# Kernel tuning notes

Hardware: AMD Instinct MI355X
Metric: run time of the kernel (lower is better)

## Reference

```python
import jax, jax.numpy as jnp
import numpy as np

B, T, D_OBS = 64, 512, 128
D_LAT, D_HID, K = 16, 256, 8
VAR = 0.0005
LOG2PI = float(np.log(2.0 * np.pi))


def _leaky(x):
    return jnp.where(x > 0, x, 0.01 * x)


def setup_inputs() -> dict:
    key = jax.random.key(0)
    ks = jax.random.split(key, 12)
    s = 0.05
    return {
        "x": jax.random.normal(ks[0], (B, T, D_OBS), jnp.float32),
        "eps": jax.random.normal(ks[1], (B, T, D_LAT), jnp.float32),
        "W1": jax.random.normal(ks[2], (D_OBS, D_HID), jnp.float32) * s,
        "b1": jnp.zeros((D_HID,), jnp.float32),
        "W2": jax.random.normal(ks[3], (D_HID, 2 * D_LAT), jnp.float32) * s,
        "b2": jnp.zeros((2 * D_LAT,), jnp.float32),
        "Wt1": jax.random.normal(ks[4], (K, D_LAT, D_HID), jnp.float32) * s,
        "bt1": jnp.zeros((K, D_HID), jnp.float32),
        "Wt2": jax.random.normal(ks[5], (K, D_HID, D_LAT), jnp.float32) * s,
        "bt2": jnp.zeros((K, D_LAT), jnp.float32),
        "Wd1": jax.random.normal(ks[6], (D_LAT, D_HID), jnp.float32) * s,
        "bd1": jnp.zeros((D_HID,), jnp.float32),
        "Wd2": jax.random.normal(ks[7], (D_HID, D_OBS), jnp.float32) * s,
        "bd2": jnp.zeros((D_OBS,), jnp.float32),
        "Q": jax.random.normal(ks[8], (K, K), jnp.float32) * 0.1,
        "pi": jax.random.normal(ks[9], (K,), jnp.float32) * 0.1,
        "init_mean": jax.random.normal(ks[10], (K, D_LAT), jnp.float32),
        "init_cov": jax.random.uniform(ks[11], (K, 1, 1), jnp.float32) * jnp.eye(D_LAT, dtype=jnp.float32)[None] * 5.0,
        "covs": jnp.tile(jnp.eye(D_LAT, dtype=jnp.float32)[None], (K, 1, 1)),
    }


def _mvn_logprob(diff, chol):
    # diff [..., K, d]; chol [K, d, d] lower Cholesky of per-state covariance
    d = chol.shape[-1]
    Linv = jax.scipy.linalg.solve_triangular(
        chol, jnp.broadcast_to(jnp.eye(d, dtype=chol.dtype), chol.shape), lower=True)
    sol = jnp.einsum('kij,...kj->...ki', Linv, diff)
    logdet = 2.0 * jnp.sum(jnp.log(jnp.diagonal(chol, axis1=-2, axis2=-1)), -1)  # [K]
    return -0.5 * (d * LOG2PI + logdet + jnp.sum(sol * sol, -1))


def _forward(x, eps, W1, b1, W2, b2, Wt1, bt1, Wt2, bt2, Wd1, bd1, Wd2, bd2,
             Q, pi, init_mean, init_cov, covs):
    Bx = x.shape[0]
    dz = init_mean.shape[-1]
    # ---- factored MLP encoder: x -> (mu, logvar); reparameterized sample ----
    h = _leaky(x @ W1 + b1)
    enc = h @ W2 + b2
    z_mu, z_log_var = enc[..., :dz], enc[..., dz:]
    z = z_mu + jnp.exp(0.5 * z_log_var) * eps                            # [B,T,dz]
    # ---- local evidence log p(z_t | z_{t-1}, s_t=k) ----
    jitter = 1e-6 * jnp.eye(dz, dtype=x.dtype)
    L0 = jnp.linalg.cholesky(init_cov @ jnp.swapaxes(init_cov, -1, -2) + jitter)
    ev1 = _mvn_logprob(z[:, 0:1, None, :] - init_mean[None, None], L0)   # [B,1,K]
    ht = jax.nn.softplus(jnp.einsum('btd,kdh->btkh', z[:, :-1], Wt1) + bt1)
    means = jnp.einsum('btkh,khd->btkd', ht, Wt2) + bt2                  # [B,T-1,K,dz]
    Lt = jnp.linalg.cholesky(covs @ jnp.swapaxes(covs, -1, -2) + jitter)
    evT = _mvn_logprob(z[:, 1:, None, :] - means, Lt)                    # [B,T-1,K]
    ev = jnp.concatenate([ev1, evT], axis=1)                             # [B,T,K]
    # ---- HMM alpha recursion in log domain (temperature=1) ----
    log_pi = jax.nn.log_softmax(pi)
    Qlog = jax.nn.log_softmax(Q, axis=-1).T                              # [new, old]
    lp0 = ev[:, 0] + log_pi
    lZ0 = jax.scipy.special.logsumexp(lp0, axis=-1)
    la0 = lp0 - lZ0[:, None]

    def step(la, ev_t):
        lp = jax.scipy.special.logsumexp(ev_t[:, :, None] + Qlog[None] + la[:, None, :], axis=-1)
        lZ = jax.scipy.special.logsumexp(lp, axis=-1)
        return lp - lZ[:, None], lZ

    _, lZs = jax.lax.scan(step, la0, jnp.moveaxis(ev[:, 1:], 1, 0))
    log_Z = lZ0 + jnp.sum(lZs, axis=0)                                   # [B]
    # ---- decoder ----
    x_hat = _leaky(z @ Wd1 + bd1) @ Wd2 + bd2
    # ---- ELBO ----
    recon = jnp.sum(-0.5 * jnp.log(2.0 * jnp.pi * VAR) - (x - x_hat) ** 2 / (2.0 * VAR)) / Bx
    logq = -0.5 * (dz * LOG2PI + jnp.sum(z_log_var, -1)
                   + jnp.sum((z - z_mu) ** 2 / jnp.exp(z_log_var), -1))
    entropy_q = -jnp.sum(logq) / Bx
    msm = jnp.sum(log_Z) / Bx
    loss = -(recon + entropy_q + msm)
    return x_hat, z, loss


def reference(x, eps, W1, b1, W2, b2, Wt1, bt1, Wt2, bt2, Wd1, bd1, Wd2, bd2,
              Q, pi, init_mean, init_cov, covs):
    return _forward(x, eps, W1, b1, W2, b2, Wt1, bt1, Wt2, bt2, Wd1, bd1, Wd2, bd2,
                    Q, pi, init_mean, init_cov, covs)
```

## Files before the change

### kernel.cpp

```cpp
#include <hip/hip_runtime.h>
#include <math.h>

#define B_SZ   64
#define T_SZ   512
#define DOBS   128
#define DLAT   16
#define DHID   256
#define K_SZ   8
#define ROWS_A 32768

#define LOG2PI_F 1.8378770664093453f
#define VAR_F    5.0e-4f

#define LINV0_OFF   16
#define LOGDET0_OFF 2064
#define LINVT_OFF   2080
#define LOGDETT_OFF 4128
#define CVEC_OFF    4224
#define WIMG_F_OFF  8192

#define EVT_W1   0
#define EVT_W2   49152
#define EVT_LINV 82944
#define ENC_W1   86016
#define ENC_W2   120832
#define DEC_W1   129280
#define DEC_W2   135424
#define WCVT_TOTAL 182272

#define Z_OUT_OFF   4194304
#define LOSS_OFF    4718592
#define PBUF_OFF  262144
#define ACC_OFF   327680

typedef __attribute__((ext_vector_type(8))) short short8;
typedef __attribute__((ext_vector_type(8))) unsigned short ush8;
typedef __attribute__((ext_vector_type(4))) float floatx4;

__device__ __forceinline__ float leakyf(float v) { return v > 0.f ? v : 0.01f * v; }
__device__ __forceinline__ unsigned short f2bf(float f) {
  union { float f; unsigned int u; } v; v.f = f;
  unsigned int lsb = (v.u >> 16) & 1;
  v.u += 0x7fffu + lsb;
  return (unsigned short)(v.u >> 16);
}
__device__ __forceinline__ unsigned int cvt_pk_bf16(float lo, float hi) {
  unsigned int r;
  asm("v_cvt_pk_bf16_f32 %0, %1, %2" : "=v"(r) : "v"(lo), "v"(hi));
  return r;
}
__device__ __forceinline__ float softplus5(float v) {
  return 0.69314718f * __log2f(1.f + exp2f(1.44269504f * v));
}
__device__ __forceinline__ int permk(int kk) {
  return (kk & ~31) | ((kk & 15) << 1) | ((kk >> 4) & 1);
}

__global__ __launch_bounds__(256) void prep_kernel(const float* __restrict__ init_cov,
                                                   const float* __restrict__ covs,
                                                   const float* __restrict__ Wt2,
                                                   const float* __restrict__ bt2,
                                                   float* __restrict__ ws,
                                                   float* __restrict__ w2l) {
  __shared__ float M[16][16];
  __shared__ float L[16][16];
  __shared__ float X[16][17];
  int job = blockIdx.x;
  const float* C = (job < 8) ? (init_cov + job * 256) : (covs + (job - 8) * 256);
  float* linv = ws + ((job < 8) ? (LINV0_OFF + job * 256) : (LINVT_OFF + (job - 8) * 256));
  float* logdet = ws + ((job < 8) ? (LOGDET0_OFF + job) : (LOGDETT_OFF + (job - 8)));
  int tid = threadIdx.x;
  if (job == 0 && tid < 4) ws[tid] = 0.f;
  int i = tid >> 4, j = tid & 15;
  {
    float s = (i == j) ? 1e-6f : 0.f;
    #pragma unroll
    for (int p = 0; p < 16; ++p) s += C[i * 16 + p] * C[j * 16 + p];
    M[i][j] = s;
  }
  __syncthreads();
  for (int c = 0; c < 16; ++c) {
    if (tid == 0) {
      float s = M[c][c];
      for (int p = 0; p < c; ++p) s -= L[c][p] * L[c][p];
      L[c][c] = sqrtf(s);
    }
    __syncthreads();
    if (tid > c && tid < 16) {
      float s = M[tid][c];
      for (int p = 0; p < c; ++p) s -= L[tid][p] * L[c][p];
      L[tid][c] = s / L[c][c];
    }
    __syncthreads();
  }
  if (tid < 16) {
    for (int r = 0; r < 16; ++r) {
      float s = (r == tid) ? 1.f : 0.f;
      for (int p = tid; p < r; ++p) s -= L[r][p] * X[p][tid];
      X[r][tid] = (r >= tid) ? s / L[r][r] : 0.f;
    }
  }
  __syncthreads();
  linv[i * 16 + j] = X[i][j];
  if (tid == 0) {
    float s = 0.f;
    for (int d = 0; d < 16; ++d) s += logf(L[d][d]);
    *logdet = 2.f * s;
  }
  if (job >= 8) {
    int k = job - 8;
    const float* wrow = Wt2 + (long)k * 4096 + tid * 16;
    float* orow = w2l + (long)k * 4096 + tid * 16;
    #pragma unroll
    for (int i2 = 0; i2 < 16; ++i2) {
      float s = 0.f;
      for (int jj = 0; jj <= i2; ++jj) s += wrow[jj] * X[i2][jj];
      orow[i2] = s;
    }
    if (tid < 16) {
      float s = 0.f;
      const float* b = bt2 + k * 16;
      for (int jj = 0; jj <= tid; ++jj) s += b[jj] * X[tid][jj];
      ws[CVEC_OFF + k * 16 + tid] = s;
    }
  }
}

__global__ __launch_bounds__(256) void wcvt_kernel(
    const float* __restrict__ Wt1, const float* __restrict__ bt1,
    const float* __restrict__ W1, const float* __restrict__ W2,
    const float* __restrict__ Wd1, const float* __restrict__ bd1,
    const float* __restrict__ Wd2,
    const float* __restrict__ ws, const float* __restrict__ w2l,
    unsigned short* __restrict__ wimg) {
  for (int e = blockIdx.x * 256 + threadIdx.x; e < WCVT_TOTAL; e += gridDim.x * 256) {
    if (e < 65536) {
      int k = e >> 13, r = e & 8191, ch = r >> 5, d = r & 31;
      if (d < 24) {
        float v = (d < 16) ? Wt1[k * 4096 + d * 256 + ch]
                           : ((d == 16) ? bt1[k * 256 + ch] : 0.f);
        wimg[EVT_W1 + k * 6144 + ch * 24 + d] = f2bf(v);
      }
    } else if (e < 98304) {
      int e2 = e - 65536; int k = e2 >> 12, r = e2 & 4095, d2 = r >> 8, h = r & 255;
      wimg[EVT_W2 + k * 4224 + d2 * 264 + permk(h)] = f2bf(w2l[(long)k * 4096 + h * 16 + d2]);
    } else if (e < 100352) {
      int e2 = e - 98304; int k = e2 >> 8, r = e2 & 255, i = r >> 4, j = r & 15;
      wimg[EVT_LINV + k * 384 + i * 24 + j] = f2bf(ws[LINVT_OFF + k * 256 + i * 16 + j]);
    } else if (e < 133120) {
      int e2 = e - 100352; int n = e2 >> 7, kk = e2 & 127;
      wimg[ENC_W1 + n * 136 + kk] = f2bf(W1[kk * 256 + n]);
    } else if (e < 141312) {
      int e2 = e - 133120; int n = e2 >> 8, kk = e2 & 255;
      wimg[ENC_W2 + n * 264 + permk(kk)] = f2bf(W2[kk * 32 + n]);
    } else if (e < 149504) {
      int e2 = e - 141312; int n = e2 >> 5, d = e2 & 31;
      if (d < 24) {
        float v = (d < 16) ? Wd1[d * 256 + n] : ((d == 16) ? bd1[n] : 0.f);
        wimg[DEC_W1 + n * 24 + d] = f2bf(v);
      }
    } else {
      int e2 = e - 149504; int kk = e2 >> 7, n = e2 & 127;
      wimg[DEC_W2 + n * 264 + permk(kk)] = f2bf(Wd2[kk * 128 + n]);
    }
  }
}

__global__ __launch_bounds__(256) void enc_kernel(
    const float* __restrict__ x, const float* __restrict__ eps,
    const float* __restrict__ b1, const float* __restrict__ b2,
    const unsigned short* __restrict__ wimg,
    float* __restrict__ z_out, float* __restrict__ ws) {
  __shared__ __align__(16) unsigned short w2t[32 * 264];
  __shared__ __align__(16) unsigned short ttile[4][16 * 56];
  __shared__ float b1s[256];
  __shared__ float sred;
  int tid = threadIdx.x;
  if (tid == 0) sred = 0.f;
  {
    const ush8* s2 = (const ush8*)(wimg + ENC_W2);
    for (int e = tid; e < 1056; e += 256) ((ush8*)w2t)[e] = s2[e];
    b1s[tid] = b1[tid];
  }
  __syncthreads();

  int wid = tid >> 6, lane = tid & 63;
  int m = lane & 15, quad = lane >> 4;
  unsigned short* tt = ttile[wid];
  const unsigned short* w1i = wimg + ENC_W1;
  long rowb = (long)blockIdx.x * 64 + wid * 16;

  short8 xa[4];
  const float* xp = x + (rowb + m) * 128 + quad * 8;
  #pragma unroll
  for (int kt = 0; kt < 4; ++kt) {
    float4 f0 = *(const float4*)(xp + kt * 32);
    float4 f1 = *(const float4*)(xp + kt * 32 + 4);
    union { unsigned int u[4]; short8 s; } cv;
    cv.u[0] = cvt_pk_bf16(f0.x, f0.y);
    cv.u[1] = cvt_pk_bf16(f0.z, f0.w);
    cv.u[2] = cvt_pk_bf16(f1.x, f1.y);
    cv.u[3] = cvt_pk_bf16(f1.z, f1.w);
    xa[kt] = cv.s;
  }
  float bm0 = b2[m], bm1 = b2[16 + m];
  floatx4 a20 = {bm0, bm0, bm0, bm0};
  floatx4 a21 = {bm1, bm1, bm1, bm1};
  #pragma unroll
  for (int cp = 0; cp < 8; ++cp) {
    floatx4 a1h[2];
    #pragma unroll
    for (int h = 0; h < 2; ++h) {
      int c = cp * 2 + h;
      float bias = b1s[c * 16 + m];
      floatx4 a1 = {bias, bias, bias, bias};
      #pragma unroll
      for (int kt = 0; kt < 4; ++kt) {
        short8 bf = *(const short8*)&w1i[(c * 16 + m) * 136 + kt * 32 + quad * 8];
        a1 = __builtin_amdgcn_mfma_f32_16x16x32_bf16(xa[kt], bf, a1, 0, 0, 0);
      }
      a1h[h] = a1;
    }
    #pragma unroll
    for (int g = 0; g < 4; ++g) {
      unsigned int p = cvt_pk_bf16(leakyf(a1h[0][g]), leakyf(a1h[1][g]));
      *(unsigned int*)&tt[(quad * 4 + g) * 56 + 2 * m] = p;
    }
    short8 ha = *(const short8*)&tt[m * 56 + quad * 8];
    short8 wb0 = *(const short8*)&w2t[m * 264 + cp * 32 + quad * 8];
    short8 wb1 = *(const short8*)&w2t[(16 + m) * 264 + cp * 32 + quad * 8];
    a20 = __builtin_amdgcn_mfma_f32_16x16x32_bf16(ha, wb0, a20, 0, 0, 0);
    a21 = __builtin_amdgcn_mfma_f32_16x16x32_bf16(ha, wb1, a21, 0, 0, 0);
  }
  float logq_acc = 0.f;
  #pragma unroll
  for (int g = 0; g < 4; ++g) {
    long row = rowb + quad * 4 + g;
    float mu = a20[g], lv = a21[g];
    float ev = eps[row * 16 + m];
    float zv = mu + __expf(0.5f * lv) * ev;
    z_out[row * 16 + m] = zv;
    float zz = zv - mu;
    logq_acc += lv + zz * zz * __expf(-lv);
  }
  #pragma unroll
  for (int off = 1; off < 64; off <<= 1) logq_acc += __shfl_xor(logq_acc, off, 64);
  if (lane == 0) atomicAdd(&sred, -0.5f * logq_acc);
  __syncthreads();
  if (tid == 0) atomicAdd(&ws[1], sred - 0.5f * 16.f * LOG2PI_F * 64.f);
}

__global__ __launch_bounds__(256, 8) void evt_kernel(
    const float* __restrict__ z, const unsigned short* __restrict__ wimg,
    const float* __restrict__ ws, float* __restrict__ evT) {
  __shared__ __align__(16) unsigned short w2t[4224];
  __shared__ __align__(16) unsigned short ttile[4][16 * 56];
  __shared__ __align__(16) unsigned short linvb[384];
  int tid = threadIdx.x;
  int k = blockIdx.y;
  {
    const ush8* s2 = (const ush8*)(wimg + EVT_W2 + k * 4224);
    for (int e = tid; e < 528; e += 256) ((ush8*)w2t)[e] = s2[e];
    if (tid < 48) ((ush8*)linvb)[tid] = ((const ush8*)(wimg + EVT_LINV + k * 384))[tid];
  }
  float logdetk = ws[LOGDETT_OFF + k];
  __syncthreads();

  int wid = tid >> 6, lane = tid & 63;
  int m = lane & 15, quad = lane >> 4;
  unsigned short* tt = ttile[wid];
  const unsigned short* w1i = wimg + EVT_W1 + k * 6144;
  float cval = ws[CVEC_OFF + k * 16 + m];

  for (int tile = 0; tile < 2; ++tile) {
    long rowb = (long)blockIdx.x * 128 + wid * 32 + tile * 16;
    short8 za = (short8)0;
    if (quad < 2) {
      const float* zp = z + (rowb + m) * 16 + quad * 8;
      float4 f0 = *(const float4*)zp;
      float4 f1 = *(const float4*)(zp + 4);
      union { unsigned int u[4]; short8 s; } cv;
      cv.u[0] = cvt_pk_bf16(f0.x, f0.y);
      cv.u[1] = cvt_pk_bf16(f0.z, f0.w);
      cv.u[2] = cvt_pk_bf16(f1.x, f1.y);
      cv.u[3] = cvt_pk_bf16(f1.z, f1.w);
      za = cv.s;
    } else if (quad == 2) {
      za[0] = (short)0x3F80;
    }
    short8 za2 = (short8)0;
    if (quad < 2) {
      long r2 = rowb + m + 1; if (r2 > 32767) r2 = 32767;
      const float* zp2 = z + r2 * 16 + quad * 8;
      float4 f0 = *(const float4*)zp2;
      float4 f1 = *(const float4*)(zp2 + 4);
      union { unsigned int u[4]; short8 s; } cv;
      cv.u[0] = cvt_pk_bf16(f0.x, f0.y);
      cv.u[1] = cvt_pk_bf16(f0.z, f0.w);
      cv.u[2] = cvt_pk_bf16(f1.x, f1.y);
      cv.u[3] = cvt_pk_bf16(f1.z, f1.w);
      za2 = cv.s;
    }
    floatx4 a2 = {cval, cval, cval, cval};
    #pragma unroll
    for (int cp = 0; cp < 8; ++cp) {
      floatx4 a1h[2];
      #pragma unroll
      for (int h = 0; h < 2; ++h) {
        int c = cp * 2 + h;
        short8 bfrag = (short8)0;
        if (quad < 3) bfrag = *(const short8*)&w1i[(c * 16 + m) * 24 + quad * 8];
        floatx4 a1 = {0.f, 0.f, 0.f, 0.f};
        a1 = __builtin_amdgcn_mfma_f32_16x16x32_bf16(za, bfrag, a1, 0, 0, 0);
        a1h[h] = a1;
      }
      #pragma unroll
      for (int g = 0; g < 4; ++g) {
        unsigned int p = cvt_pk_bf16(softplus5(a1h[0][g]), softplus5(a1h[1][g]));
        *(unsigned int*)&tt[(quad * 4 + g) * 56 + 2 * m] = p;
      }
      short8 ha = *(const short8*)&tt[m * 56 + quad * 8];
      short8 wb = *(const short8*)&w2t[m * 264 + cp * 32 + quad * 8];
      a2 = __builtin_amdgcn_mfma_f32_16x16x32_bf16(ha, wb, a2, 0, 0, 0);
    }
    short8 lb = (short8)0;
    if (quad < 2) lb = *(const short8*)&linvb[m * 24 + quad * 8];
    floatx4 a3 = {0.f, 0.f, 0.f, 0.f};
    a3 = __builtin_amdgcn_mfma_f32_16x16x32_bf16(za2, lb, a3, 0, 0, 0);
    #pragma unroll
    for (int g = 0; g < 4; ++g) {
      float v = a3[g] - a2[g];
      v = v * v;
      v += __shfl_xor(v, 1, 64);
      v += __shfl_xor(v, 2, 64);
      v += __shfl_xor(v, 4, 64);
      v += __shfl_xor(v, 8, 64);
      long grow = rowb + quad * 4 + g;
      if (m == 0 && (grow & 511) != 511) {
        long r1 = grow + 1;
        evT[(r1 >> 9) * 4096 + (long)k * 512 + (r1 & 511)] =
            -0.5f * (16.f * LOG2PI_F + logdetk + v);
      }
    }
  }
}

__global__ __launch_bounds__(256) void hmm_scan(const float* __restrict__ Q,
                                                const float* __restrict__ evT,
                                                float* __restrict__ pbuf,
                                                float* __restrict__ accbuf) {
  int tid = threadIdx.x;
  int wid = tid >> 6, lane = tid & 63;
  int job = blockIdx.x * 4 + wid;
  int b = job >> 4, c = job & 15;
  int i = lane >> 3, j = lane & 7;

  float qp[8];
  #pragma unroll
  for (int p = 0; p < 8; ++p) {
    float mr = Q[p * 8 + 0];
    #pragma unroll
    for (int cc = 1; cc < 8; ++cc) mr = fmaxf(mr, Q[p * 8 + cc]);
    float rs = 0.f;
    #pragma unroll
    for (int cc = 0; cc < 8; ++cc) rs += __expf(Q[p * 8 + cc] - mr);
    qp[p] = __expf(Q[p * 8 + i] - mr) / rs;
  }
  float qself;
  {
    float mr = Q[j * 8 + 0];
    #pragma unroll
    for (int cc = 1; cc < 8; ++cc) mr = fmaxf(mr, Q[j * 8 + cc]);
    float rs = 0.f;
    #pragma unroll
    for (int cc = 0; cc < 8; ++cc) rs += __expf(Q[j * 8 + cc] - mr);
    qself = __expf(Q[j * 8 + i] - mr) / rs;
  }

  int t0 = 1 + c * 32;
  int L = (c == 15) ? 31 : 32;
  const float* evI = evT + (long)b * 4096 + (long)i * 512 + t0;

  float f[32];
  float accm = 0.f;
  #pragma unroll
  for (int s = 0; s < 32; ++s) {
    float e = (s < L) ? evI[s] : 0.f;
    float m = e;
    m = fmaxf(m, __shfl_xor(m, 8, 64));
    m = fmaxf(m, __shfl_xor(m, 16, 64));
    m = fmaxf(m, __shfl_xor(m, 32, 64));
    f[s] = __expf(e - m);
    if (s < L) accm += m;
  }

  float P = f[0] * qself;
  #pragma unroll
  for (int s = 1; s < 32; ++s) {
    if (s < L) {
      float a0 = __shfl(P, j,      64);
      float a1 = __shfl(P, 8 + j,  64);
      float a2 = __shfl(P, 16 + j, 64);
      float a3 = __shfl(P, 24 + j, 64);
      float a4 = __shfl(P, 32 + j, 64);
      float a5 = __shfl(P, 40 + j, 64);
      float a6 = __shfl(P, 48 + j, 64);
      float a7 = __shfl(P, 56 + j, 64);
      float sv = ((qp[0] * a0 + qp[1] * a1) + (qp[2] * a2 + qp[3] * a3))
               + ((qp[4] * a4 + qp[5] * a5) + (qp[6] * a6 + qp[7] * a7));
      P = f[s] * sv;
    }
    if ((s & 7) == 7) {
      float mx = P;
      mx = fmaxf(mx, __shfl_xor(mx, 1, 64));
      mx = fmaxf(mx, __shfl_xor(mx, 2, 64));
      mx = fmaxf(mx, __shfl_xor(mx, 4, 64));
      mx = fmaxf(mx, __shfl_xor(mx, 8, 64));
      mx = fmaxf(mx, __shfl_xor(mx, 16, 64));
      mx = fmaxf(mx, __shfl_xor(mx, 32, 64));
      mx = fmaxf(mx, 1e-30f);
      P = P / mx;
      accm += __logf(mx);
    }
  }
  pbuf[(long)job * 64 + lane] = P;
  if (lane == 0) accbuf[job] = accm;
}

__global__ __launch_bounds__(512) void hmm_comb(const float* __restrict__ pi,
                                                const float* __restrict__ z,
                                                const float* __restrict__ init_mean,
                                                const float* __restrict__ pbuf,
                                                const float* __restrict__ accbuf,
                                                float* __restrict__ ws) {
  int tid = threadIdx.x;
  int wid = tid >> 6, lane = tid & 63;
  int b = blockIdx.x * 8 + wid;
  int j = lane & 7;

  float mp = pi[0];
  #pragma unroll
  for (int cc = 1; cc < 8; ++cc) mp = fmaxf(mp, pi[cc]);
  float sp = 0.f;
  #pragma unroll
  for (int cc = 0; cc < 8; ++cc) sp += __expf(pi[cc] - mp);
  float lpi = pi[j] - mp - __logf(sp);

  const float* zr = z + (long)b * 8192;
  const float* linv = ws + LINV0_OFF + j * 256;
  float diff[16];
  #pragma unroll
  for (int d = 0; d < 16; ++d) diff[d] = zr[d] - init_mean[j * 16 + d];
  float quad0 = 0.f;
  #pragma unroll
  for (int i2 = 0; i2 < 16; ++i2) {
    float s = 0.f;
    #pragma unroll
    for (int jj = 0; jj < 16; ++jj) s += linv[i2 * 16 + jj] * diff[jj];
    quad0 += s * s;
  }
  float ev0 = -0.5f * (16.f * LOG2PI_F + ws[LOGDET0_OFF + j] + quad0);

  float lp0 = ev0 + lpi;
  float m0 = lp0;
  m0 = fmaxf(m0, __shfl_xor(m0, 1, 64));
  m0 = fmaxf(m0, __shfl_xor(m0, 2, 64));
  m0 = fmaxf(m0, __shfl_xor(m0, 4, 64));
  float u = __expf(lp0 - m0);
  double acc = (double)m0;

  #pragma unroll
  for (int c = 0; c < 16; ++c) {
    float P = pbuf[((long)b * 16 + c) * 64 + lane];
    float contrib = P * u;
    contrib += __shfl_xor(contrib, 1, 64);
    contrib += __shfl_xor(contrib, 2, 64);
    contrib += __shfl_xor(contrib, 4, 64);
    u = __shfl(contrib, j * 9, 64);
    float mxu = u;
    mxu = fmaxf(mxu, __shfl_xor(mxu, 1, 64));
    mxu = fmaxf(mxu, __shfl_xor(mxu, 2, 64));
    mxu = fmaxf(mxu, __shfl_xor(mxu, 4, 64));
    mxu = fmaxf(mxu, 1e-30f);
    u = u / mxu;
    acc += (double)(__logf(mxu) + accbuf[b * 16 + c]);
  }
  float su = u;
  su += __shfl_xor(su, 1, 64);
  su += __shfl_xor(su, 2, 64);
  su += __shfl_xor(su, 4, 64);
  float logZ = (float)(acc + (double)__logf(su));
  if (lane == 0) atomicAdd(&ws[2], logZ);
}

__global__ __launch_bounds__(256) void dec_kernel(
    const float* __restrict__ x, const float* __restrict__ z,
    const float* __restrict__ bd2,
    const unsigned short* __restrict__ wimg,
    float* __restrict__ xhat, float* __restrict__ ws) {
  __shared__ __align__(16) unsigned short w1t[6144];
  __shared__ __align__(16) unsigned short ttile[4][16 * 56];
  __shared__ float bd2s[128];
  __shared__ float sred;
  int tid = threadIdx.x;
  if (tid == 0) sred = 0.f;
  {
    const ush8* s1 = (const ush8*)(wimg + DEC_W1);
    for (int e = tid; e < 768; e += 256) ((ush8*)w1t)[e] = s1[e];
    if (tid < 128) bd2s[tid] = bd2[tid];
  }
  __syncthreads();

  int wid = tid >> 6, lane = tid & 63;
  int m = lane & 15, quad = lane >> 4;
  unsigned short* tt = ttile[wid];
  const unsigned short* w2i = wimg + DEC_W2;
  long rowb = (long)blockIdx.x * 64 + wid * 16;

  short8 za = (short8)0;
  if (quad < 2) {
    const float* zp = z + (rowb + m) * 16 + quad * 8;
    float4 f0 = *(const float4*)zp;
    float4 f1 = *(const float4*)(zp + 4);
    union { unsigned int u[4]; short8 s; } cv;
    cv.u[0] = cvt_pk_bf16(f0.x, f0.y);
    cv.u[1] = cvt_pk_bf16(f0.z, f0.w);
    cv.u[2] = cvt_pk_bf16(f1.x, f1.y);
    cv.u[3] = cvt_pk_bf16(f1.z, f1.w);
    za = cv.s;
  } else if (quad == 2) {
    za[0] = (short)0x3F80;
  }
  floatx4 a2[8];
  #pragma unroll
  for (int c2 = 0; c2 < 8; ++c2) {
    float bv = bd2s[c2 * 16 + m];
    a2[c2] = (floatx4){bv, bv, bv, bv};
  }
  #pragma unroll
  for (int cp = 0; cp < 8; ++cp) {
    floatx4 a1h[2];
    #pragma unroll
    for (int h = 0; h < 2; ++h) {
      int c = cp * 2 + h;
      short8 bfrag = (short8)0;
      if (quad < 3) bfrag = *(const short8*)&w1t[(c * 16 + m) * 24 + quad * 8];
      floatx4 a1 = {0.f, 0.f, 0.f, 0.f};
      a1 = __builtin_amdgcn_mfma_f32_16x16x32_bf16(za, bfrag, a1, 0, 0, 0);
      a1h[h] = a1;
    }
    #pragma unroll
    for (int g = 0; g < 4; ++g) {
      unsigned int p = cvt_pk_bf16(leakyf(a1h[0][g]), leakyf(a1h[1][g]));
      *(unsigned int*)&tt[(quad * 4 + g) * 56 + 2 * m] = p;
    }
    short8 ha = *(const short8*)&tt[m * 56 + quad * 8];
    #pragma unroll
    for (int c2 = 0; c2 < 8; ++c2) {
      short8 wb = *(const short8*)&w2i[(c2 * 16 + m) * 264 + cp * 32 + quad * 8];
      a2[c2] = __builtin_amdgcn_mfma_f32_16x16x32_bf16(ha, wb, a2[c2], 0, 0, 0);
    }
  }
  const float C0 = -0.5f * logf(6.2831853071795864f * VAR_F);
  float rsum = 0.f;
  #pragma unroll
  for (int c2 = 0; c2 < 8; ++c2) {
    int col = c2 * 16 + m;
    #pragma unroll
    for (int g = 0; g < 4; ++g) {
      long row = rowb + quad * 4 + g;
      float xh = a2[c2][g];
      xhat[row * 128 + col] = xh;
      float dd = x[row * 128 + col] - xh;
      rsum += C0 - dd * dd * (0.5f / VAR_F);
    }
  }
  #pragma unroll
  for (int off = 1; off < 64; off <<= 1) rsum += __shfl_xor(rsum, off, 64);
  if (lane == 0) atomicAdd(&sred, rsum);
  __syncthreads();
  if (tid == 0) atomicAdd(&ws[0], sred);
}

__global__ void fin_kernel(const float* __restrict__ ws, float* __restrict__ out) {
  float loss = -((ws[0] - ws[1] + ws[2]) * (1.f / 64.f));
  out[LOSS_OFF] = loss;
}

extern "C" void kernel_launch(void* const* d_in, const int* in_sizes, int n_in,
                              void* d_out, int out_size, void* d_ws, size_t ws_size,
                              hipStream_t stream) {
  (void)in_sizes; (void)n_in; (void)out_size; (void)ws_size;
  const float* x   = (const float*)d_in[0];
  const float* eps = (const float*)d_in[1];
  const float* W1  = (const float*)d_in[2];
  const float* b1  = (const float*)d_in[3];
  const float* W2  = (const float*)d_in[4];
  const float* b2  = (const float*)d_in[5];
  const float* Wt1 = (const float*)d_in[6];
  const float* bt1 = (const float*)d_in[7];
  const float* Wt2 = (const float*)d_in[8];
  const float* bt2 = (const float*)d_in[9];
  const float* Wd1 = (const float*)d_in[10];
  const float* bd1 = (const float*)d_in[11];
  const float* Wd2 = (const float*)d_in[12];
  const float* bd2 = (const float*)d_in[13];
  const float* Q   = (const float*)d_in[14];
  const float* pi  = (const float*)d_in[15];
  const float* im  = (const float*)d_in[16];
  const float* ic  = (const float*)d_in[17];
  const float* cv  = (const float*)d_in[18];
  float* out = (float*)d_out;
  float* ws  = (float*)d_ws;
  float* z_out = out + Z_OUT_OFF;
  float* evT  = out;
  float* pbuf = out + PBUF_OFF;
  float* accb = out + ACC_OFF;
  unsigned short* wimg = (unsigned short*)(ws + WIMG_F_OFF);

  prep_kernel<<<16, 256, 0, stream>>>(ic, cv, Wt2, bt2, ws, pbuf);
  wcvt_kernel<<<144, 256, 0, stream>>>(Wt1, bt1, W1, W2, Wd1, bd1, Wd2, ws, pbuf, wimg);
  enc_kernel<<<512, 256, 0, stream>>>(x, eps, b1, b2, wimg, z_out, ws);
  evt_kernel<<<dim3(256, 8), 256, 0, stream>>>(z_out, wimg, ws, evT);
  hmm_scan<<<256, 256, 0, stream>>>(Q, evT, pbuf, accb);
  hmm_comb<<<8, 512, 0, stream>>>(pi, z_out, im, pbuf, accb, ws);
  dec_kernel<<<512, 256, 0, stream>>>(x, z_out, bd2, wimg, out, ws);
  fin_kernel<<<1, 1, 0, stream>>>(ws, out);
}
```

Measured before the change: 240.6 us.

## Fuse HMM scan and combine kernels, fold final loss into decoder

Merges the chunked HMM forward scan and its cross-chunk combine into one kernel, with one 1024-thread block per batch element that keeps the chunk results in shared memory instead of a global buffer. Removes the separate final loss kernel by having the last decoder block, found through an atomic counter, compute the loss. It also swaps the base-2 softplus formula for __logf/__expf. This cuts two launches and a global round trip, but the HMM stage now runs only 64 blocks, and in the combine step only one of the 16 waves per block does work.

```diff
diff --git a/kernel.cpp b/kernel.cpp
--- a/kernel.cpp
+++ b/kernel.cpp
@@ -31,7 +31,6 @@
 #define Z_OUT_OFF   4194304
 #define LOSS_OFF    4718592
 #define PBUF_OFF  262144
-#define ACC_OFF   327680
 
 typedef __attribute__((ext_vector_type(8))) short short8;
 typedef __attribute__((ext_vector_type(8))) unsigned short ush8;
@@ -49,8 +48,8 @@
   asm("v_cvt_pk_bf16_f32 %0, %1, %2" : "=v"(r) : "v"(lo), "v"(hi));
   return r;
 }
-__device__ __forceinline__ float softplus5(float v) {
-  return 0.69314718f * __log2f(1.f + exp2f(1.44269504f * v));
+__device__ __forceinline__ float softplus_fast(float v) {
+  return __logf(1.f + __expf(v));
 }
 __device__ __forceinline__ int permk(int kk) {
   return (kk & ~31) | ((kk & 15) << 1) | ((kk >> 4) & 1);
@@ -70,7 +69,7 @@
   float* linv = ws + ((job < 8) ? (LINV0_OFF + job * 256) : (LINVT_OFF + (job - 8) * 256));
   float* logdet = ws + ((job < 8) ? (LOGDET0_OFF + job) : (LOGDETT_OFF + (job - 8)));
   int tid = threadIdx.x;
-  if (job == 0 && tid < 4) ws[tid] = 0.f;
+  if (job == 0 && tid < 8) ws[tid] = 0.f;
   int i = tid >> 4, j = tid & 15;
   {
     float s = (i == j) ? 1e-6f : 0.f;
@@ -316,7 +315,7 @@
       }
       #pragma unroll
       for (int g = 0; g < 4; ++g) {
-        unsigned int p = cvt_pk_bf16(softplus5(a1h[0][g]), softplus5(a1h[1][g]));
+        unsigned int p = cvt_pk_bf16(softplus_fast(a1h[0][g]), softplus_fast(a1h[1][g]));
         *(unsigned int*)&tt[(quad * 4 + g) * 56 + 2 * m] = p;
       }
       short8 ha = *(const short8*)&tt[m * 56 + quad * 8];
@@ -345,14 +344,15 @@
   }
 }
 
-__global__ __launch_bounds__(256) void hmm_scan(const float* __restrict__ Q,
-                                                const float* __restrict__ evT,
-                                                float* __restrict__ pbuf,
-                                                float* __restrict__ accbuf) {
+__global__ __launch_bounds__(1024) void hmm_fused(
+    const float* __restrict__ Q, const float* __restrict__ pi,
+    const float* __restrict__ z, const float* __restrict__ init_mean,
+    const float* __restrict__ evT, float* __restrict__ ws) {
+  __shared__ float sP[16][64];
+  __shared__ float sacc[16];
   int tid = threadIdx.x;
-  int wid = tid >> 6, lane = tid & 63;
-  int job = blockIdx.x * 4 + wid;
-  int b = job >> 4, c = job & 15;
+  int c = tid >> 6, lane = tid & 63;
+  int b = blockIdx.x;
   int i = lane >> 3, j = lane & 7;
 
   float qp[8];
@@ -423,74 +423,65 @@
       accm += __logf(mx);
     }
   }
-  pbuf[(long)job * 64 + lane] = P;
-  if (lane == 0) accbuf[job] = accm;
-}
-
-__global__ __launch_bounds__(512) void hmm_comb(const float* __restrict__ pi,
-                                                const float* __restrict__ z,
-                                                const float* __restrict__ init_mean,
-                                                const float* __restrict__ pbuf,
-                                                const float* __restrict__ accbuf,
-                                                float* __restrict__ ws) {
-  int tid = threadIdx.x;
-  int wid = tid >> 6, lane = tid & 63;
-  int b = blockIdx.x * 8 + wid;
-  int j = lane & 7;
-
-  float mp = pi[0];
-  #pragma unroll
-  for (int cc = 1; cc < 8; ++cc) mp = fmaxf(mp, pi[cc]);
-  float sp = 0.f;
-  #pragma unroll
-  for (int cc = 0; cc < 8; ++cc) sp += __expf(pi[cc] - mp);
-  float lpi = pi[j] - mp - __logf(sp);
-
-  const float* zr = z + (long)b * 8192;
-  const float* linv = ws + LINV0_OFF + j * 256;
-  float diff[16];
-  #pragma unroll
-  for (int d = 0; d < 16; ++d) diff[d] = zr[d] - init_mean[j * 16 + d];
-  float quad0 = 0.f;
-  #pragma unroll
-  for (int i2 = 0; i2 < 16; ++i2) {
-    float s = 0.f;
-    #pragma unroll
-    for (int jj = 0; jj < 16; ++jj) s += linv[i2 * 16 + jj] * diff[jj];
-    quad0 += s * s;
-  }
-  float ev0 = -0.5f * (16.f * LOG2PI_F + ws[LOGDET0_OFF + j] + quad0);
-
-  float lp0 = ev0 + lpi;
-  float m0 = lp0;
-  m0 = fmaxf(m0, __shfl_xor(m0, 1, 64));
-  m0 = fmaxf(m0, __shfl_xor(m0, 2, 64));
-  m0 = fmaxf(m0, __shfl_xor(m0, 4, 64));
-  float u = __expf(lp0 - m0);
-  double acc = (double)m0;
-
-  #pragma unroll
-  for (int c = 0; c < 16; ++c) {
-    float P = pbuf[((long)b * 16 + c) * 64 + lane];
-    float contrib = P * u;
-    contrib += __shfl_xor(contrib, 1, 64);
-    contrib += __shfl_xor(contrib, 2, 64);
-    contrib += __shfl_xor(contrib, 4, 64);
-    u = __shfl(contrib, j * 9, 64);
-    float mxu = u;
-    mxu = fmaxf(mxu, __shfl_xor(mxu, 1, 64));
-    mxu = fmaxf(mxu, __shfl_xor(mxu, 2, 64));
-    mxu = fmaxf(mxu, __shfl_xor(mxu, 4, 64));
-    mxu = fmaxf(mxu, 1e-30f);
-    u = u / mxu;
-    acc += (double)(__logf(mxu) + accbuf[b * 16 + c]);
-  }
-  float su = u;
-  su += __shfl_xor(su, 1, 64);
-  su += __shfl_xor(su, 2, 64);
-  su += __shfl_xor(su, 4, 64);
-  float logZ = (float)(acc + (double)__logf(su));
-  if (lane == 0) atomicAdd(&ws[2], logZ);
+  sP[c][lane] = P;
+  if (lane == 0) sacc[c] = accm;
+  __syncthreads();
+
+  if (c == 0) {
+    float mp = pi[0];
+    #pragma unroll
+    for (int cc = 1; cc < 8; ++cc) mp = fmaxf(mp, pi[cc]);
+    float sp = 0.f;
+    #pragma unroll
+    for (int cc = 0; cc < 8; ++cc) sp += __expf(pi[cc] - mp);
+    float lpi = pi[j] - mp - __logf(sp);
+
+    const float* zr = z + (long)b * 8192;
+    const float* linv = ws + LINV0_OFF + j * 256;
+    float diff[16];
+    #pragma unroll
+    for (int d = 0; d < 16; ++d) diff[d] = zr[d] - init_mean[j * 16 + d];
+    float quad0 = 0.f;
+    #pragma unroll
+    for (int i2 = 0; i2 < 16; ++i2) {
+      float s = 0.f;
+      #pragma unroll
+      for (int jj = 0; jj < 16; ++jj) s += linv[i2 * 16 + jj] * diff[jj];
+      quad0 += s * s;
+    }
+    float ev0 = -0.5f * (16.f * LOG2PI_F + ws[LOGDET0_OFF + j] + quad0);
+
+    float lp0 = ev0 + lpi;
+    float m0 = lp0;
+    m0 = fmaxf(m0, __shfl_xor(m0, 1, 64));
+    m0 = fmaxf(m0, __shfl_xor(m0, 2, 64));
+    m0 = fmaxf(m0, __shfl_xor(m0, 4, 64));
+    float u = __expf(lp0 - m0);
+    double acc = (double)m0;
+
+    #pragma unroll
+    for (int cc2 = 0; cc2 < 16; ++cc2) {
+      float Pc = sP[cc2][lane];
+      float contrib = Pc * u;
+      contrib += __shfl_xor(contrib, 1, 64);
+      contrib += __shfl_xor(contrib, 2, 64);
+      contrib += __shfl_xor(contrib, 4, 64);
+      u = __shfl(contrib, j * 9, 64);
+      float mxu = u;
+      mxu = fmaxf(mxu, __shfl_xor(mxu, 1, 64));
+      mxu = fmaxf(mxu, __shfl_xor(mxu, 2, 64));
+      mxu = fmaxf(mxu, __shfl_xor(mxu, 4, 64));
+      mxu = fmaxf(mxu, 1e-30f);
+      u = u / mxu;
+      acc += (double)(__logf(mxu) + sacc[cc2]);
+    }
+    float su = u;
+    su += __shfl_xor(su, 1, 64);
+    su += __shfl_xor(su, 2, 64);
+    su += __shfl_xor(su, 4, 64);
+    float logZ = (float)(acc + (double)__logf(su));
+    if (lane == 0) atomicAdd(&ws[2], logZ);
+  }
 }
 
 __global__ __launch_bounds__(256) void dec_kernel(
@@ -579,12 +570,17 @@
   for (int off = 1; off < 64; off <<= 1) rsum += __shfl_xor(rsum, off, 64);
   if (lane == 0) atomicAdd(&sred, rsum);
   __syncthreads();
-  if (tid == 0) atomicAdd(&ws[0], sred);
-}
-
-__global__ void fin_kernel(const float* __restrict__ ws, float* __restrict__ out) {
-  float loss = -((ws[0] - ws[1] + ws[2]) * (1.f / 64.f));
-  out[LOSS_OFF] = loss;
+  if (tid == 0) {
+    atomicAdd(&ws[0], sred);
+    __threadfence();
+    unsigned int t = atomicAdd((unsigned int*)(ws + 4), 1u);
+    if (t == gridDim.x - 1) {
+      __threadfence();
+      float recon = atomicAdd(&ws[0], 0.f);
+      float loss = -((recon - ws[1] + ws[2]) * (1.f / 64.f));
+      xhat[LOSS_OFF] = loss;
+    }
+  }
 }
 
 extern "C" void kernel_launch(void* const* d_in, const int* in_sizes, int n_in,
@@ -614,16 +610,13 @@
   float* ws  = (float*)d_ws;
   float* z_out = out + Z_OUT_OFF;
   float* evT  = out;
-  float* pbuf = out + PBUF_OFF;
-  float* accb = out + ACC_OFF;
+  float* w2l  = out + PBUF_OFF;
   unsigned short* wimg = (unsigned short*)(ws + WIMG_F_OFF);
 
-  prep_kernel<<<16, 256, 0, stream>>>(ic, cv, Wt2, bt2, ws, pbuf);
-  wcvt_kernel<<<144, 256, 0, stream>>>(Wt1, bt1, W1, W2, Wd1, bd1, Wd2, ws, pbuf, wimg);
+  prep_kernel<<<16, 256, 0, stream>>>(ic, cv, Wt2, bt2, ws, w2l);
+  wcvt_kernel<<<144, 256, 0, stream>>>(Wt1, bt1, W1, W2, Wd1, bd1, Wd2, ws, w2l, wimg);
   enc_kernel<<<512, 256, 0, stream>>>(x, eps, b1, b2, wimg, z_out, ws);
   evt_kernel<<<dim3(256, 8), 256, 0, stream>>>(z_out, wimg, ws, evT);
-  hmm_scan<<<256, 256, 0, stream>>>(Q, evT, pbuf, accb);
-  hmm_comb<<<8, 512, 0, stream>>>(pi, z_out, im, pbuf, accb, ws);
+  hmm_fused<<<64, 1024, 0, stream>>>(Q, pi, z_out, im, evT, ws);
   dec_kernel<<<512, 256, 0, stream>>>(x, z_out, bd2, wimg, out, ws);
-  fin_kernel<<<1, 1, 0, stream>>>(ws, out);
-}
+}
```

Measured after the change: 245.2 us. No clear change (+1.9%).
